# Kernel optimization log

Hardware: AMD Instinct MI355X
Metric: run time of the kernel (lower is better)

Reference implementation:

```python
import jax, jax.numpy as jnp
import numpy as np

EMBED_DIM = 1024
NUM_HEADS = 16
HEAD_DIM = EMBED_DIM // NUM_HEADS


def setup_inputs() -> dict:
    key = jax.random.key(0)
    ks = jax.random.split(key, 10)
    s = 1.0 / np.sqrt(EMBED_DIM)
    x = jax.random.normal(ks[0], (2, 2048, EMBED_DIM), dtype=jnp.float32)
    Wq = jax.random.uniform(ks[1], (EMBED_DIM, EMBED_DIM), jnp.float32, -s, s)
    bq = jax.random.uniform(ks[2], (EMBED_DIM,), jnp.float32, -s, s)
    Wk = jax.random.uniform(ks[3], (EMBED_DIM, EMBED_DIM), jnp.float32, -s, s)
    bk = jax.random.uniform(ks[4], (EMBED_DIM,), jnp.float32, -s, s)
    Wv = jax.random.uniform(ks[5], (EMBED_DIM, EMBED_DIM), jnp.float32, -s, s)
    bv = jax.random.uniform(ks[6], (EMBED_DIM,), jnp.float32, -s, s)
    Wo = jax.random.uniform(ks[7], (EMBED_DIM, EMBED_DIM), jnp.float32, -s, s)
    bo = jax.random.uniform(ks[8], (EMBED_DIM,), jnp.float32, -s, s)
    return {"x": x, "Wq": Wq, "bq": bq, "Wk": Wk, "bk": bk,
            "Wv": Wv, "bv": bv, "Wo": Wo, "bo": bo}


def reference(x, Wq, bq, Wk, bk, Wv, bv, Wo, bo):
    b, s, e = x.shape
    h, d = NUM_HEADS, HEAD_DIM
    scale = d ** -0.5
    # projections (torch Linear: x @ W.T + b; here W stored as [in, out])
    q = (x @ Wq + bq).reshape(b, s, h, d)
    k = (x @ Wk + bk).reshape(b, s, h, d)
    v = (x @ Wv + bv).reshape(b, s, h, d)
    logits = jnp.einsum('bqhd,bkhd->bhqk', q, k) * scale
    causal = jnp.tril(jnp.ones((s, s), dtype=bool))  # keep lower triangle
    logits = jnp.where(causal, logits, -jnp.inf)
    attn = jax.nn.softmax(logits, axis=-1)
    out = jnp.einsum('bhqk,bkhd->bqhd', attn, v).reshape(b, s, e)
    return out @ Wo + bo
```

## Files before the change

kernel.cpp:

```cpp
#include <hip/hip_runtime.h>


#define EMB 1024
#define SEQ 2048
#define NB 2
#define NH 16
#define HD 64

#define QSCALE 0.18033688011112042f

typedef float f32x4 __attribute__((ext_vector_type(4)));
typedef float floatx4 __attribute__((ext_vector_type(4)));
typedef short short8 __attribute__((ext_vector_type(8)));
typedef __bf16 bf16x8 __attribute__((ext_vector_type(8)));
typedef __bf16 bf16x2 __attribute__((ext_vector_type(2)));
typedef unsigned short ushortx4 __attribute__((ext_vector_type(4)));
typedef unsigned int uintx4 __attribute__((ext_vector_type(4)));

__device__ __forceinline__ unsigned short bf16u(float f) {
  __bf16 h = (__bf16)f;
  return __builtin_bit_cast(unsigned short, h);
}

__device__ __forceinline__ unsigned pkbf(float lo, float hi) {
  bf16x2 v;
  v[0] = (__bf16)lo;
  v[1] = (__bf16)hi;
  return __builtin_bit_cast(unsigned, v);
}

__device__ __forceinline__ f32x4 mfma16(short8 a, short8 b, f32x4 c) {
  return __builtin_amdgcn_mfma_f32_16x16x32_bf16(
      __builtin_bit_cast(bf16x8, a), __builtin_bit_cast(bf16x8, b), c, 0, 0, 0);
}

__device__ __forceinline__ void gload16(const void* g, void* lds) {
  __builtin_amdgcn_global_load_lds(
      (const __attribute__((address_space(1))) unsigned int*)g,
      (__attribute__((address_space(3))) unsigned int*)lds, 16, 0, 0);
}

__global__ __launch_bounds__(256) void cvt_x_kernel(
    const float* __restrict__ x, unsigned short* __restrict__ out) {
  const int idx = (blockIdx.x * 256 + threadIdx.x) * 4;
  floatx4 v = *(const floatx4*)(x + idx);
  ushortx4 o;
  #pragma unroll
  for (int i = 0; i < 4; ++i) o[i] = bf16u(v[i]);
  *(ushortx4*)(out + idx) = o;
}

__global__ __launch_bounds__(256) void cvt_w4_kernel(
    const float* __restrict__ W0, const float* __restrict__ W1,
    const float* __restrict__ W2, const float* __restrict__ W3,
    unsigned short* __restrict__ T0, unsigned short* __restrict__ T1,
    unsigned short* __restrict__ T2, unsigned short* __restrict__ T3) {
  __shared__ unsigned short tile[32][33];
  const int z = blockIdx.z;
  const float* W = (z == 0) ? W0 : (z == 1) ? W1 : (z == 2) ? W2 : W3;
  unsigned short* WT = (z == 0) ? T0 : (z == 1) ? T1 : (z == 2) ? T2 : T3;
  const int k0 = blockIdx.x * 32, n0 = blockIdx.y * 32;
  const int t = threadIdx.x;
  const int r = t >> 3, c = (t & 7) * 4;
  floatx4 v = *(const floatx4*)(W + (k0 + r) * EMB + n0 + c);
  #pragma unroll
  for (int i = 0; i < 4; ++i) tile[r][c + i] = bf16u(v[i]);
  __syncthreads();
  ushortx4 o;
  #pragma unroll
  for (int i = 0; i < 4; ++i) o[i] = tile[c + i][r];
  *(ushortx4*)(WT + (n0 + r) * EMB + k0 + c) = o;
}

#define GEMM_KLOOP(OP1, OP2)                                                 \
    for (int kk = 0; kk < 64; kk += 32) {                                    \
      short8 a[4], b[4];                                                     \
      _Pragma("unroll")                                                      \
      for (int i = 0; i < 4; ++i)                                            \
        a[i] = *(const short8*)(As + (wr * 64 + i * 16 + ln) * 64 + kk + g * 8); \
      _Pragma("unroll")                                                      \
      for (int j = 0; j < 4; ++j)                                            \
        b[j] = *(const short8*)(Bs + (wc * 64 + j * 16 + ln) * 64 + kk + g * 8); \
      _Pragma("unroll")                                                      \
      for (int i = 0; i < 4; ++i)                                            \
        _Pragma("unroll")                                                    \
        for (int j = 0; j < 4; ++j)                                          \
          acc[i][j] = mfma16(OP1, OP2, acc[i][j]);                           \
    }

__global__ __launch_bounds__(256) void gemm_qkv_kernel(
    const unsigned short* __restrict__ Xb,
    const unsigned short* __restrict__ W0, const unsigned short* __restrict__ W1,
    const unsigned short* __restrict__ W2,
    const float* __restrict__ b0, const float* __restrict__ b1,
    const float* __restrict__ b2,
    unsigned short* __restrict__ Qo, unsigned short* __restrict__ Ko,
    unsigned short* __restrict__ Vo) {
  __shared__ __align__(16) unsigned short As[128 * 64];
  __shared__ __align__(16) unsigned short Bs[128 * 64];
  const int z = blockIdx.z;
  const unsigned short* Wt = (z == 0) ? W0 : ((z == 1) ? W1 : W2);
  const float* bias = (z == 0) ? b0 : ((z == 1) ? b1 : b2);
  const bool sw = (z != 2);
  const int m0 = blockIdx.y * 128, n0 = blockIdx.x * 128;
  const int tid = threadIdx.x, l = tid & 63, w = tid >> 6;
  const int g = l >> 4, ln = l & 15;
  const int wr = w >> 1, wc = w & 1;

  f32x4 acc[4][4];
  #pragma unroll
  for (int i = 0; i < 4; ++i)
    #pragma unroll
    for (int j = 0; j < 4; ++j) acc[i][j] = (f32x4){0.f, 0.f, 0.f, 0.f};

  for (int kt = 0; kt < 16; ++kt) {
    const int kb = kt * 64;
    #pragma unroll
    for (int it = 0; it < 4; ++it) {
      const int chunk = w * 4 + it;
      const int lin = chunk * 64 + l;
      const int row = lin >> 3, col = (lin & 7) * 8;
      gload16(Xb + (m0 + row) * EMB + kb + col, (char*)As + chunk * 1024);
      gload16(Wt + (n0 + row) * EMB + kb + col, (char*)Bs + chunk * 1024);
    }
    __syncthreads();
    if (sw) {
      GEMM_KLOOP(b[j], a[i])
    } else {
      GEMM_KLOOP(a[i], b[j])
    }
    __syncthreads();
  }

  const int mb = m0 + wr * 64, nb = n0 + wc * 64;
  if (sw) {
    unsigned short* dst = (z == 0) ? Qo : Ko;
    const float osc = (z == 0) ? QSCALE : 1.0f;
    #pragma unroll
    for (int j = 0; j < 4; ++j) {
      const int n = nb + j * 16 + 4 * g;
      floatx4 bv_ = *(const floatx4*)(bias + n);
      const int h = n >> 6, d = n & 63;
      #pragma unroll
      for (int i = 0; i < 4; ++i) {
        const int m = mb + i * 16 + ln;
        const int bb = m >> 11, ss = m & 2047;
        ushortx4 o;
        #pragma unroll
        for (int e = 0; e < 4; ++e) o[e] = bf16u((acc[i][j][e] + bv_[e]) * osc);
        *(ushortx4*)(dst + ((bb * NH + h) * SEQ + ss) * HD + d) = o;
      }
    }
  } else {
    #pragma unroll
    for (int j = 0; j < 4; ++j) {
      const int n = nb + j * 16 + ln;
      const float bgain = bias[n];
      const int h = n >> 6, d = n & 63;
      #pragma unroll
      for (int i = 0; i < 4; ++i) {
        const int mf = mb + i * 16 + 4 * g;
        const int bb = mf >> 11, ss = mf & 2047;
        ushortx4 o;
        #pragma unroll
        for (int e = 0; e < 4; ++e) o[e] = bf16u(acc[i][j][e] + bgain);
        *(ushortx4*)(Vo + ((bb * NH + h) * HD + d) * SEQ + ss) = o;
      }
    }
  }
}

__global__ __launch_bounds__(512) void attn_kernel(
    const unsigned short* __restrict__ Q, const unsigned short* __restrict__ K,
    const unsigned short* __restrict__ Vt, unsigned short* __restrict__ O) {
  __shared__ __align__(16) unsigned short Kt[2][128 * 64];
  __shared__ __align__(16) unsigned short Vl[2][64 * 128];
  const int id = blockIdx.x;
  const int bh = id & 31;
  const int grp = id >> 5;
  const int T = (grp < 8) ? (15 - grp) : (grp - 8);
  const int h = bh & 15, b = bh >> 4;
  const int tid = threadIdx.x, l = tid & 63, w = tid >> 6;
  const int g = l >> 4, ln = l & 15;
  const size_t baseQK = (size_t)bh * SEQ * HD;
  const size_t baseV = (size_t)bh * HD * SEQ;
  const int xr = ln & 7;
  const int srcA = ((g & 1) << 5) + ln;
  const int srcB = srcA + 16;
  const bool hi = (g >> 1) != 0;

  const int kr0 = (2 * w) * 8 + (l >> 3), kr1 = (2 * w + 1) * 8 + (l >> 3);
  const int kc0 = (l & 7) ^ (kr0 & 7), kc1 = (l & 7) ^ (kr1 & 7);
  const int vr0 = (2 * w) * 4 + (l >> 4), vr1 = (2 * w + 1) * 4 + (l >> 4);
  const int vc0 = (l & 15) ^ (vr0 & 15), vc1 = (l & 15) ^ (vr1 & 15);

  const int nkt = T + 1;
  const int qw = T * 128 + w * 16;

  gload16(K + baseQK + (size_t)kr0 * HD + kc0 * 8,
          (char*)&Kt[0][0] + (2 * w) * 1024);
  gload16(K + baseQK + (size_t)kr1 * HD + kc1 * 8,
          (char*)&Kt[0][0] + (2 * w + 1) * 1024);
  gload16(Vt + baseV + (size_t)vr0 * SEQ + vc0 * 8,
          (char*)&Vl[0][0] + (2 * w) * 1024);
  gload16(Vt + baseV + (size_t)vr1 * SEQ + vc1 * 8,
          (char*)&Vl[0][0] + (2 * w + 1) * 1024);

  const int qrow = qw + ln;
  short8 qf0 = *(const short8*)(Q + baseQK + (size_t)qrow * HD + g * 8);
  short8 qf1 = *(const short8*)(Q + baseQK + (size_t)qrow * HD + 32 + g * 8);

  float m_run = -1e30f, l_run = 0.f;
  f32x4 acc[4];
  #pragma unroll
  for (int dj = 0; dj < 4; ++dj) acc[dj] = (f32x4){0.f, 0.f, 0.f, 0.f};

  #pragma unroll 1
  for (int kt = 0; kt < nkt; ++kt) {
    const int cur = kt & 1;
    const bool has_next = (kt + 1 < nkt);
    if (has_next) {
      const int nxt = cur ^ 1;
      const size_t kof = (size_t)(kt + 1) * 128;
      gload16(K + baseQK + (kof + kr0) * HD + kc0 * 8,
              (char*)&Kt[nxt][0] + (2 * w) * 1024);
      gload16(K + baseQK + (kof + kr1) * HD + kc1 * 8,
              (char*)&Kt[nxt][0] + (2 * w + 1) * 1024);
      gload16(Vt + baseV + (size_t)vr0 * SEQ + kof + vc0 * 8,
              (char*)&Vl[nxt][0] + (2 * w) * 1024);
      gload16(Vt + baseV + (size_t)vr1 * SEQ + kof + vc1 * 8,
              (char*)&Vl[nxt][0] + (2 * w + 1) * 1024);
      asm volatile("s_waitcnt vmcnt(4)" ::: "memory");
    } else {
      asm volatile("s_waitcnt vmcnt(0)" ::: "memory");
    }
    __builtin_amdgcn_s_barrier();

    const bool last = (kt == T);
    const int jmax = last ? w : 7;

    f32x4 sv[8];
    #pragma unroll
    for (int j = 0; j < 8; ++j)
      sv[j] = (f32x4){-1e30f, -1e30f, -1e30f, -1e30f};
    __builtin_amdgcn_s_setprio(1);
    #pragma unroll
    for (int j = 0; j < 8; ++j) {
      if (j <= jmax) {
        f32x4 t = (f32x4){0.f, 0.f, 0.f, 0.f};
        short8 kf0 = *(const short8*)(
            &Kt[cur][(j * 16 + ln) * 64 + ((g ^ xr) * 8)]);
        t = mfma16(kf0, qf0, t);
        short8 kf1 = *(const short8*)(
            &Kt[cur][(j * 16 + ln) * 64 + (((4 + g) ^ xr) * 8)]);
        t = mfma16(kf1, qf1, t);
        if (last && j == w) {
          #pragma unroll
          for (int e = 0; e < 4; ++e)
            sv[j][e] = (4 * g + e <= ln) ? t[e] : -1e30f;
        } else {
          sv[j] = t;
        }
      }
    }
    __builtin_amdgcn_s_setprio(0);

    float tj[8];
    #pragma unroll
    for (int j = 0; j < 8; ++j)
      tj[j] = fmaxf(fmaxf(sv[j][0], sv[j][1]), fmaxf(sv[j][2], sv[j][3]));
    float tm = fmaxf(fmaxf(fmaxf(tj[0], tj[1]), fmaxf(tj[2], tj[3])),
                     fmaxf(fmaxf(tj[4], tj[5]), fmaxf(tj[6], tj[7])));
    tm = fmaxf(tm, __shfl_xor(tm, 16));
    tm = fmaxf(tm, __shfl_xor(tm, 32));
    const float nm = fmaxf(m_run, tm);
    const float al = exp2f(m_run - nm);
    m_run = nm;

    unsigned pk[8][2];
    float rs = 0.f;
    #pragma unroll
    for (int j = 0; j < 8; ++j) {
      const float p0 = exp2f(sv[j][0] - nm), p1 = exp2f(sv[j][1] - nm);
      const float p2 = exp2f(sv[j][2] - nm), p3 = exp2f(sv[j][3] - nm);
      rs += (p0 + p1) + (p2 + p3);
      pk[j][0] = pkbf(p0, p1);
      pk[j][1] = pkbf(p2, p3);
    }
    rs += __shfl_xor(rs, 16);
    rs += __shfl_xor(rs, 32);
    l_run = l_run * al + rs;
    #pragma unroll
    for (int dj = 0; dj < 4; ++dj) acc[dj] *= al;

    const int ksmax = (jmax >> 1) + 1;
    short8 pf[4];
    #pragma unroll
    for (int ks = 0; ks < 4; ++ks) {
      if (ks < ksmax) {
        unsigned a0 = __shfl(pk[2 * ks][0], srcA);
        unsigned a1 = __shfl(pk[2 * ks][1], srcA);
        unsigned a2 = __shfl(pk[2 * ks][0], srcB);
        unsigned a3 = __shfl(pk[2 * ks][1], srcB);
        unsigned b0 = __shfl(pk[2 * ks + 1][0], srcA);
        unsigned b1 = __shfl(pk[2 * ks + 1][1], srcA);
        unsigned b2 = __shfl(pk[2 * ks + 1][0], srcB);
        unsigned b3 = __shfl(pk[2 * ks + 1][1], srcB);
        uintx4 u;
        u[0] = hi ? b0 : a0; u[1] = hi ? b1 : a1;
        u[2] = hi ? b2 : a2; u[3] = hi ? b3 : a3;
        pf[ks] = __builtin_bit_cast(short8, u);
      }
    }

    __builtin_amdgcn_s_setprio(1);
    #pragma unroll
    for (int dj = 0; dj < 4; ++dj) {
      #pragma unroll
      for (int ks = 0; ks < 4; ++ks) {
        if (ks < ksmax) {
          short8 vb = *(const short8*)(
              &Vl[cur][(dj * 16 + ln) * 128 + (((ks * 4 + g) ^ ln) * 8)]);
          acc[dj] = mfma16(vb, pf[ks], acc[dj]);
        }
      }
    }
    __builtin_amdgcn_s_setprio(0);

    asm volatile("" ::: "memory");
    __builtin_amdgcn_s_barrier();
  }

  const float inv = 1.f / l_run;
  const size_t orow = ((size_t)b * SEQ + qw + ln) * EMB + h * HD;
  #pragma unroll
  for (int dj = 0; dj < 4; ++dj) {
    ushortx4 o;
    #pragma unroll
    for (int e = 0; e < 4; ++e) o[e] = bf16u(acc[dj][e] * inv);
    *(ushortx4*)(O + orow + dj * 16 + 4 * g) = o;
  }
}

__global__ __launch_bounds__(256) void gemm_o_kernel(
    const unsigned short* __restrict__ Ab, const unsigned short* __restrict__ Wt,
    const float* __restrict__ bias, float* __restrict__ out) {
  __shared__ __align__(16) unsigned short As[128 * 64];
  __shared__ __align__(16) unsigned short Bs[128 * 64];
  const int m0 = blockIdx.y * 128, n0 = blockIdx.x * 128;
  const int tid = threadIdx.x, l = tid & 63, w = tid >> 6;
  const int g = l >> 4, ln = l & 15;
  const int wr = w >> 1, wc = w & 1;

  f32x4 acc[4][4];
  #pragma unroll
  for (int i = 0; i < 4; ++i)
    #pragma unroll
    for (int j = 0; j < 4; ++j) acc[i][j] = (f32x4){0.f, 0.f, 0.f, 0.f};

  for (int kt = 0; kt < 16; ++kt) {
    const int kb = kt * 64;
    #pragma unroll
    for (int it = 0; it < 4; ++it) {
      const int chunk = w * 4 + it;
      const int lin = chunk * 64 + l;
      const int row = lin >> 3, col = (lin & 7) * 8;
      gload16(Ab + (m0 + row) * EMB + kb + col, (char*)As + chunk * 1024);
      gload16(Wt + (n0 + row) * EMB + kb + col, (char*)Bs + chunk * 1024);
    }
    __syncthreads();
    GEMM_KLOOP(b[j], a[i])
    __syncthreads();
  }

  const int mb = m0 + wr * 64, nb = n0 + wc * 64;
  #pragma unroll
  for (int j = 0; j < 4; ++j) {
    const int n = nb + j * 16 + 4 * g;
    floatx4 bv_ = *(const floatx4*)(bias + n);
    #pragma unroll
    for (int i = 0; i < 4; ++i) {
      const int m = mb + i * 16 + ln;
      floatx4 o = acc[i][j] + bv_;
      *(floatx4*)(out + (size_t)m * EMB + n) = o;
    }
  }
}

extern "C" void kernel_launch(void* const* d_in, const int* in_sizes, int n_in,
                              void* d_out, int out_size, void* d_ws, size_t ws_size,
                              hipStream_t stream) {
  const float* x  = (const float*)d_in[0];
  const float* Wq = (const float*)d_in[1];
  const float* bq = (const float*)d_in[2];
  const float* Wk = (const float*)d_in[3];
  const float* bk = (const float*)d_in[4];
  const float* Wv = (const float*)d_in[5];
  const float* bv = (const float*)d_in[6];
  const float* Wo = (const float*)d_in[7];
  const float* bo = (const float*)d_in[8];
  float* out = (float*)d_out;

  char* ws = (char*)d_ws;
  unsigned short* Xb  = (unsigned short*)(ws);
  unsigned short* WqT = (unsigned short*)(ws + 8388608);
  unsigned short* WkT = (unsigned short*)(ws + 10485760);
  unsigned short* WvT = (unsigned short*)(ws + 12582912);
  unsigned short* WoT = (unsigned short*)(ws + 14680064);
  unsigned short* Qb  = (unsigned short*)(ws + 16777216);
  unsigned short* Kb  = (unsigned short*)(ws + 25165824);
  unsigned short* Vtb = (unsigned short*)(ws + 33554432);
  unsigned short* Ao  = Xb;

  hipLaunchKernelGGL(cvt_x_kernel, dim3(4096), dim3(256), 0, stream, x, Xb);
  hipLaunchKernelGGL(cvt_w4_kernel, dim3(32, 32, 4), dim3(256), 0, stream,
                     Wq, Wk, Wv, Wo, WqT, WkT, WvT, WoT);
  hipLaunchKernelGGL(gemm_qkv_kernel, dim3(8, 32, 3), dim3(256), 0, stream,
                     Xb, WqT, WkT, WvT, bq, bk, bv, Qb, Kb, Vtb);
  hipLaunchKernelGGL(attn_kernel, dim3(512), dim3(512), 0, stream,
                     Qb, Kb, Vtb, Ao);
  hipLaunchKernelGGL(gemm_o_kernel, dim3(8, 32), dim3(256), 0, stream,
                     Ao, WoT, bo, out);
}
```

Baseline: 162.1 us.

## Double-buffer LDS tiles in QKV and output projection GEMMs

Both projection GEMMs now keep two shared-memory tile buffers and issue the async global-to-LDS loads for the next K tile before computing on the current one. Explicit vmcnt waits and raw barriers replace __syncthreads, so memory latency can overlap with MFMA work. This doubles LDS use per block to 64 KB, which may cut occupancy. It also relies on the hand-written vmcnt count matching the number of outstanding loads.

```diff
diff --git a/kernel.cpp b/kernel.cpp
--- a/kernel.cpp
+++ b/kernel.cpp
@@ -88,6 +88,21 @@
           acc[i][j] = mfma16(OP1, OP2, acc[i][j]);                           \
     }
 
+#define GEMM_STAGE(Aptr, Bptr, kt_, buf_)                                    \
+    do {                                                                     \
+      const int kb_ = (kt_) * 64;                                            \
+      _Pragma("unroll")                                                      \
+      for (int it = 0; it < 4; ++it) {                                       \
+        const int chunk = w * 4 + it;                                        \
+        const int lin = chunk * 64 + l;                                      \
+        const int row = lin >> 3, col = (lin & 7) * 8;                       \
+        gload16(Aptr + (m0 + row) * EMB + kb_ + col,                         \
+                (char*)&AsB[buf_][0] + chunk * 1024);                        \
+        gload16(Bptr + (n0 + row) * EMB + kb_ + col,                         \
+                (char*)&BsB[buf_][0] + chunk * 1024);                        \
+      }                                                                      \
+    } while (0)
+
 __global__ __launch_bounds__(256) void gemm_qkv_kernel(
     const unsigned short* __restrict__ Xb,
     const unsigned short* __restrict__ W0, const unsigned short* __restrict__ W1,
@@ -96,8 +111,8 @@
     const float* __restrict__ b2,
     unsigned short* __restrict__ Qo, unsigned short* __restrict__ Ko,
     unsigned short* __restrict__ Vo) {
-  __shared__ __align__(16) unsigned short As[128 * 64];
-  __shared__ __align__(16) unsigned short Bs[128 * 64];
+  __shared__ __align__(16) unsigned short AsB[2][128 * 64];
+  __shared__ __align__(16) unsigned short BsB[2][128 * 64];
   const int z = blockIdx.z;
   const unsigned short* Wt = (z == 0) ? W0 : ((z == 1) ? W1 : W2);
   const float* bias = (z == 0) ? b0 : ((z == 1) ? b1 : b2);
@@ -113,23 +128,26 @@
     #pragma unroll
     for (int j = 0; j < 4; ++j) acc[i][j] = (f32x4){0.f, 0.f, 0.f, 0.f};
 
+  GEMM_STAGE(Xb, Wt, 0, 0);
+  #pragma unroll 1
   for (int kt = 0; kt < 16; ++kt) {
-    const int kb = kt * 64;
-    #pragma unroll
-    for (int it = 0; it < 4; ++it) {
-      const int chunk = w * 4 + it;
-      const int lin = chunk * 64 + l;
-      const int row = lin >> 3, col = (lin & 7) * 8;
-      gload16(Xb + (m0 + row) * EMB + kb + col, (char*)As + chunk * 1024);
-      gload16(Wt + (n0 + row) * EMB + kb + col, (char*)Bs + chunk * 1024);
-    }
-    __syncthreads();
+    const int cur = kt & 1;
+    if (kt + 1 < 16) {
+      GEMM_STAGE(Xb, Wt, kt + 1, cur ^ 1);
+      asm volatile("s_waitcnt vmcnt(8)" ::: "memory");
+    } else {
+      asm volatile("s_waitcnt vmcnt(0)" ::: "memory");
+    }
+    __builtin_amdgcn_s_barrier();
+    const unsigned short* As = &AsB[cur][0];
+    const unsigned short* Bs = &BsB[cur][0];
     if (sw) {
       GEMM_KLOOP(b[j], a[i])
     } else {
       GEMM_KLOOP(a[i], b[j])
     }
-    __syncthreads();
+    asm volatile("" ::: "memory");
+    __builtin_amdgcn_s_barrier();
   }
 
   const int mb = m0 + wr * 64, nb = n0 + wc * 64;
@@ -345,8 +363,8 @@
 __global__ __launch_bounds__(256) void gemm_o_kernel(
     const unsigned short* __restrict__ Ab, const unsigned short* __restrict__ Wt,
     const float* __restrict__ bias, float* __restrict__ out) {
-  __shared__ __align__(16) unsigned short As[128 * 64];
-  __shared__ __align__(16) unsigned short Bs[128 * 64];
+  __shared__ __align__(16) unsigned short AsB[2][128 * 64];
+  __shared__ __align__(16) unsigned short BsB[2][128 * 64];
   const int m0 = blockIdx.y * 128, n0 = blockIdx.x * 128;
   const int tid = threadIdx.x, l = tid & 63, w = tid >> 6;
   const int g = l >> 4, ln = l & 15;
@@ -358,19 +376,22 @@
     #pragma unroll
     for (int j = 0; j < 4; ++j) acc[i][j] = (f32x4){0.f, 0.f, 0.f, 0.f};
 
+  GEMM_STAGE(Ab, Wt, 0, 0);
+  #pragma unroll 1
   for (int kt = 0; kt < 16; ++kt) {
-    const int kb = kt * 64;
-    #pragma unroll
-    for (int it = 0; it < 4; ++it) {
-      const int chunk = w * 4 + it;
-      const int lin = chunk * 64 + l;
-      const int row = lin >> 3, col = (lin & 7) * 8;
-      gload16(Ab + (m0 + row) * EMB + kb + col, (char*)As + chunk * 1024);
-      gload16(Wt + (n0 + row) * EMB + kb + col, (char*)Bs + chunk * 1024);
-    }
-    __syncthreads();
+    const int cur = kt & 1;
+    if (kt + 1 < 16) {
+      GEMM_STAGE(Ab, Wt, kt + 1, cur ^ 1);
+      asm volatile("s_waitcnt vmcnt(8)" ::: "memory");
+    } else {
+      asm volatile("s_waitcnt vmcnt(0)" ::: "memory");
+    }
+    __builtin_amdgcn_s_barrier();
+    const unsigned short* As = &AsB[cur][0];
+    const unsigned short* Bs = &BsB[cur][0];
     GEMM_KLOOP(b[j], a[i])
-    __syncthreads();
+    asm volatile("" ::: "memory");
+    __builtin_amdgcn_s_barrier();
   }
 
   const int mb = m0 + wr * 64, nb = n0 + wc * 64;
```

Result: no change. 161.7 us (-0.2%).
